# Kernel tuning notes

Measured on AMD Instinct MI355X. Metric: run time of the kernel, lower is better.

Reference implementation:

```python
import jax, jax.numpy as jnp
import numpy as np

N = 50000   # nodes
E = 800000  # edges
IN, H, OUT = 64, 512, 128


def _lin_init(key, out_dim, in_dim):
    kw, kb = jax.random.split(key)
    bound = 1.0 / np.sqrt(in_dim)
    W = jax.random.uniform(kw, (out_dim, in_dim), jnp.float32, -bound, bound)
    b = jax.random.uniform(kb, (out_dim,), jnp.float32, -bound, bound)
    return W, b


def setup_inputs() -> dict:
    key = jax.random.key(0)
    ks = jax.random.split(key, 10)
    x = jax.random.normal(ks[0], (N, IN), jnp.float32)
    edge_index = jax.random.randint(ks[1], (2, E), 0, N, jnp.int64)
    W_s1, b_s1 = _lin_init(ks[2], H, IN)
    W_s2, b_s2 = _lin_init(ks[3], H, H)
    W_s3, b_s3 = _lin_init(ks[4], H, H)
    W_s4, b_s4 = _lin_init(ks[5], H, H)
    W_m1, b_m1 = _lin_init(ks[6], OUT, H)
    W_m2, b_m2 = _lin_init(ks[7], OUT, OUT)
    W_l1, b_l1 = _lin_init(ks[8], OUT, H)
    W_l2, b_l2 = _lin_init(ks[9], OUT, OUT)
    return {"x": x, "edge_index": edge_index,
            "W_s1": W_s1, "b_s1": b_s1, "W_s2": W_s2, "b_s2": b_s2,
            "W_s3": W_s3, "b_s3": b_s3, "W_s4": W_s4, "b_s4": b_s4,
            "W_m1": W_m1, "b_m1": b_m1, "W_m2": W_m2, "b_m2": b_m2,
            "W_l1": W_l1, "b_l1": b_l1, "W_l2": W_l2, "b_l2": b_l2}


def _aggregate(h, src, dst):
    # GINConv with default eps=0: (1+eps)*x + sum_{j in N(i)} x_j
    return h + jax.ops.segment_sum(h[src], dst, num_segments=N)


def reference(x, edge_index,
              W_s1, b_s1, W_s2, b_s2, W_s3, b_s3, W_s4, b_s4,
              W_m1, b_m1, W_m2, b_m2, W_l1, b_l1, W_l2, b_l2):
    src, dst = edge_index[0], edge_index[1]
    lrelu = lambda v: jax.nn.leaky_relu(v, 0.1)

    def mlp_shared(h):
        h = lrelu(h @ W_s1.T + b_s1)
        h = lrelu(h @ W_s2.T + b_s2)
        h = lrelu(h @ W_s3.T + b_s3)
        return h @ W_s4.T + b_s4

    def mlp_mu(h):
        return jax.nn.relu(h @ W_m1.T + b_m1) @ W_m2.T + b_m2

    def mlp_logvar(h):
        return jax.nn.relu(h @ W_l1.T + b_l1) @ W_l2.T + b_l2

    h = jax.nn.relu(mlp_shared(_aggregate(x, src, dst)))
    mu = mlp_mu(_aggregate(h, src, dst))
    logvar = mlp_logvar(_aggregate(h, src, dst))
    return (mu, logvar)
```

## Files before the change

kernel.cpp:

```cpp
#include <hip/hip_runtime.h>
#include <hip/hip_bf16.h>
#include <stdint.h>

#define N_NODES 50000
#define N_PAD   50048
#define E_EDGES 800000
#define MT      391

typedef __bf16 bf16x8 __attribute__((ext_vector_type(8)));
typedef __bf16 bf16x4 __attribute__((ext_vector_type(4)));
typedef float  f32x4  __attribute__((ext_vector_type(4)));

__global__ void count_deg(const int* __restrict__ ei, int* __restrict__ cnt) {
    int e = blockIdx.x * blockDim.x + threadIdx.x;
    if (e < E_EDGES) atomicAdd(&cnt[ei[E_EDGES + e]], 1);
}

#define SCAN_B 1024
__global__ void scan_block(const int* __restrict__ cnt, int* __restrict__ ptr,
                           int* __restrict__ bsum, int n) {
    __shared__ int buf[SCAN_B];
    int i = blockIdx.x * SCAN_B + threadIdx.x;
    int v = (i < n) ? cnt[i] : 0;
    buf[threadIdx.x] = v;
    __syncthreads();
    #pragma unroll
    for (int off = 1; off < SCAN_B; off <<= 1) {
        int t = (threadIdx.x >= (unsigned)off) ? buf[threadIdx.x - off] : 0;
        __syncthreads();
        buf[threadIdx.x] += t;
        __syncthreads();
    }
    if (i < n) ptr[i] = buf[threadIdx.x] - v;
    if (threadIdx.x == SCAN_B - 1) bsum[blockIdx.x] = buf[SCAN_B - 1];
}

__global__ void scan_bsums(const int* __restrict__ bsum, int* __restrict__ boff,
                           int nb, int* __restrict__ total_out) {
    __shared__ int buf[SCAN_B];
    int v = ((int)threadIdx.x < nb) ? bsum[threadIdx.x] : 0;
    buf[threadIdx.x] = v;
    __syncthreads();
    #pragma unroll
    for (int off = 1; off < SCAN_B; off <<= 1) {
        int t = (threadIdx.x >= (unsigned)off) ? buf[threadIdx.x - off] : 0;
        __syncthreads();
        buf[threadIdx.x] += t;
        __syncthreads();
    }
    if ((int)threadIdx.x < nb) boff[threadIdx.x] = buf[threadIdx.x] - v;
    if (threadIdx.x == SCAN_B - 1) *total_out = buf[SCAN_B - 1];
}

__global__ void scan_add(int* __restrict__ ptr, const int* __restrict__ boff, int n) {
    int i = blockIdx.x * SCAN_B + threadIdx.x;
    if (i < n) ptr[i] += boff[blockIdx.x];
}

__global__ void fill_csr(const int* __restrict__ ei, const int* __restrict__ ptr,
                         int* __restrict__ cursor, int* __restrict__ col) {
    int e = blockIdx.x * blockDim.x + threadIdx.x;
    if (e < E_EDGES) {
        int dst = ei[E_EDGES + e];
        int pos = ptr[dst] + atomicAdd(&cursor[dst], 1);
        col[pos] = ei[e];
    }
}

#define XN      3200000
#define WTOT    983040
__global__ void cvt_all(const float* __restrict__ x,
                        const float* __restrict__ Ws1, const float* __restrict__ Ws2,
                        const float* __restrict__ Ws3, const float* __restrict__ Ws4,
                        const float* __restrict__ Wm1, const float* __restrict__ Wl1,
                        const float* __restrict__ Wm2, const float* __restrict__ Wl2,
                        __bf16* __restrict__ xb, __bf16* __restrict__ wbuf) {
    int i = blockIdx.x * blockDim.x + threadIdx.x;
    if (i < XN) { xb[i] = (__bf16)x[i]; return; }
    int j = i - XN;
    if (j >= WTOT) return;
    const float* s; int o;
    if      (j <  32768) { s = Ws1; o = j; }
    else if (j < 294912) { s = Ws2; o = j -  32768; }
    else if (j < 557056) { s = Ws3; o = j - 294912; }
    else if (j < 819200) { s = Ws4; o = j - 557056; }
    else if (j < 884736) { s = Wm1; o = j - 819200; }
    else if (j < 950272) { s = Wl1; o = j - 884736; }
    else if (j < 966656) { s = Wm2; o = j - 950272; }
    else                 { s = Wl2; o = j - 966656; }
    wbuf[j] = (__bf16)s[o];
}

__global__ __launch_bounds__(256) void agg0_gather(
    const __bf16* __restrict__ xb, const int* __restrict__ ptr,
    const int* __restrict__ col, __bf16* __restrict__ out) {
    int node = blockIdx.x * 4 + (threadIdx.x >> 6);
    int lane = threadIdx.x & 63;
    int g    = lane >> 3;
    int f0   = (lane & 7) << 3;
    if (node >= N_PAD) return;
    long o = (long)node * 64 + f0;
    if (node >= N_NODES) {
        if (g == 0) {
            bf16x8 z;
            #pragma unroll
            for (int i = 0; i < 8; ++i) z[i] = (__bf16)0.0f;
            *(bf16x8*)&out[o] = z;
        }
        return;
    }
    float a[8];
    #pragma unroll
    for (int i = 0; i < 8; ++i) a[i] = 0.0f;
    if (g == 0) {
        bf16x8 s = *(const bf16x8*)&xb[o];
        #pragma unroll
        for (int i = 0; i < 8; ++i) a[i] = (float)s[i];
    }
    int e0 = ptr[node], e1 = ptr[node + 1];
    int e = e0;
    for (; e + 16 <= e1; e += 16) {
        int c0 = col[e + g];
        int c1 = col[e + 8 + g];
        bf16x8 v0 = *(const bf16x8*)&xb[(c0 << 6) + f0];
        bf16x8 v1 = *(const bf16x8*)&xb[(c1 << 6) + f0];
        #pragma unroll
        for (int i = 0; i < 8; ++i) a[i] += (float)v0[i] + (float)v1[i];
    }
    int rem = e1 - e;
    if (rem > 0) {
        int u0 = (g < rem) ? g : 0;        float m0 = (g < rem) ? 1.0f : 0.0f;
        int i1 = g + 8;
        int u1 = (i1 < rem) ? i1 : 0;      float m1 = (i1 < rem) ? 1.0f : 0.0f;
        int c0 = col[e + u0];
        int c1 = col[e + u1];
        bf16x8 v0 = *(const bf16x8*)&xb[(c0 << 6) + f0];
        bf16x8 v1 = *(const bf16x8*)&xb[(c1 << 6) + f0];
        #pragma unroll
        for (int i = 0; i < 8; ++i) a[i] += m0 * (float)v0[i] + m1 * (float)v1[i];
    }
    #pragma unroll
    for (int i = 0; i < 8; ++i) {
        a[i] += __shfl_xor(a[i], 8, 64);
        a[i] += __shfl_xor(a[i], 16, 64);
        a[i] += __shfl_xor(a[i], 32, 64);
    }
    if (g == 0) {
        bf16x8 r;
        #pragma unroll
        for (int i = 0; i < 8; ++i) r[i] = (__bf16)a[i];
        *(bf16x8*)&out[o] = r;
    }
}

__global__ __launch_bounds__(256) void aggt_gather(
    const __bf16* __restrict__ t, const int* __restrict__ ptr,
    const int* __restrict__ col, const float* __restrict__ b_m1,
    const float* __restrict__ b_l1, __bf16* __restrict__ p) {
    int node = blockIdx.x * 8 + (threadIdx.x >> 5);
    if (node >= N_NODES) return;
    int hl = threadIdx.x & 31;
    int f0 = hl << 3;
    float a[8];
    {
        bf16x8 s = *(const bf16x8*)&t[((long)node << 8) + f0];
        #pragma unroll
        for (int i = 0; i < 8; ++i) a[i] = (float)s[i];
    }
    int e0 = ptr[node], e1 = ptr[node + 1];
    int e = e0;
    for (; e + 8 <= e1; e += 8) {
        int c[8];
        #pragma unroll
        for (int u = 0; u < 8; ++u) c[u] = col[e + u];
        bf16x8 v[8];
        #pragma unroll
        for (int u = 0; u < 8; ++u) v[u] = *(const bf16x8*)&t[((long)c[u] << 8) + f0];
        #pragma unroll
        for (int u = 0; u < 8; ++u)
            #pragma unroll
            for (int i = 0; i < 8; ++i) a[i] += (float)v[u][i];
    }
    int rem = e1 - e;
    if (rem > 0) {
        #pragma unroll
        for (int u = 0; u < 7; ++u) {
            int   uu = (u < rem) ? u : 0;
            float m  = (u < rem) ? 1.0f : 0.0f;
            int   cc = col[e + uu];
            bf16x8 v = *(const bf16x8*)&t[((long)cc << 8) + f0];
            #pragma unroll
            for (int i = 0; i < 8; ++i) a[i] += m * (float)v[i];
        }
    }
    const float* bp = (f0 < 128) ? (b_m1 + f0) : (b_l1 + (f0 - 128));
    f32x4 b0 = *(const f32x4*)bp;
    f32x4 b1 = *(const f32x4*)(bp + 4);
    bf16x8 r;
    #pragma unroll
    for (int i = 0; i < 4; ++i) r[i]     = (__bf16)fmaxf(a[i]     + b0[i], 0.0f);
    #pragma unroll
    for (int i = 0; i < 4; ++i) r[4 + i] = (__bf16)fmaxf(a[4 + i] + b1[i], 0.0f);
    *(bf16x8*)&p[((long)node << 8) + f0] = r;
}

__device__ __forceinline__ void gl_lds16(const __bf16* g, __bf16* l) {
    __builtin_amdgcn_global_load_lds(
        (const __attribute__((address_space(1))) uint32_t*)g,
        (__attribute__((address_space(3))) uint32_t*)l, 16, 0, 0);
}

__device__ __forceinline__ void stage_w(const __bf16* __restrict__ W, int K, int k0,
                                        __bf16* __restrict__ buf, int nrows,
                                        int wid, int lane) {
    int ipw = nrows >> 7;
    int r16 = lane >> 2, sl = lane & 3;
    #pragma unroll
    for (int i = 0; i < 4; ++i) {
        if (i < ipw) {
            int cc = wid * ipw + i;
            int r  = cc * 16 + r16;
            int kt = sl ^ ((r >> 1) & 3);
            gl_lds16(W + (long)r * K + k0 + kt * 8, buf + cc * 512);
        }
    }
}

template <int NI>
__device__ __forceinline__ void chunk_mfma(const __bf16* __restrict__ sAct,
    const __bf16* __restrict__ buf, int c, int rA, int q, int wncol,
    f32x4 (&acc)[4][NI]) {
    const int g   = c * 4 + q;
    const int sla = ((g & 56) | ((g & 7) ^ (rA & 7))) << 3;
    bf16x8 af[4], bfr[NI];
    #pragma unroll
    for (int mi = 0; mi < 4; ++mi)
        af[mi] = *(const bf16x8*)&sAct[(mi * 16 + rA) * 512 + sla];
    #pragma unroll
    for (int ni = 0; ni < NI; ++ni) {
        int wr = wncol + ni * 16 + rA;
        bfr[ni] = *(const bf16x8*)&buf[wr * 32 + ((q ^ ((wr >> 1) & 3)) << 3)];
    }
    #pragma unroll
    for (int mi = 0; mi < 4; ++mi)
        #pragma unroll
        for (int ni = 0; ni < NI; ++ni)
            acc[mi][ni] = __builtin_amdgcn_mfma_f32_16x16x32_bf16(
                af[mi], bfr[ni], acc[mi][ni], 0, 0, 0);
}

__device__ __forceinline__ void chunk_mfma_a0(const __bf16* __restrict__ act0,
    const __bf16* __restrict__ buf, int c, int rA, int q, int wncol,
    f32x4 (&acc)[4][4]) {
    const int g   = c * 4 + q;
    const int sla = (g ^ (rA & 7)) << 3;
    bf16x8 af[4], bfr[4];
    #pragma unroll
    for (int mi = 0; mi < 4; ++mi)
        af[mi] = *(const bf16x8*)&act0[(mi * 16 + rA) * 64 + sla];
    #pragma unroll
    for (int ni = 0; ni < 4; ++ni) {
        int wr = wncol + ni * 16 + rA;
        bfr[ni] = *(const bf16x8*)&buf[wr * 32 + ((q ^ ((wr >> 1) & 3)) << 3)];
    }
    #pragma unroll
    for (int mi = 0; mi < 4; ++mi)
        #pragma unroll
        for (int ni = 0; ni < 4; ++ni)
            acc[mi][ni] = __builtin_amdgcn_mfma_f32_16x16x32_bf16(
                af[mi], bfr[ni], acc[mi][ni], 0, 0, 0);
}

template <int ACTn>
__device__ __forceinline__ void writeback_act(__bf16* __restrict__ sAct,
    f32x4 (&acc)[4][4], const float* __restrict__ bias,
    int wn, int ccol, int crow) {
    float bv[4];
    #pragma unroll
    for (int ni = 0; ni < 4; ++ni) bv[ni] = bias[wn + ni * 16 + ccol];
    #pragma unroll
    for (int mi = 0; mi < 4; ++mi)
        #pragma unroll
        for (int ni = 0; ni < 4; ++ni) {
            int cc = wn + ni * 16 + ccol;
            int g  = cc >> 3;
            #pragma unroll
            for (int p = 0; p < 4; ++p) {
                int rr = mi * 16 + crow + p;
                float v = acc[mi][ni][p] + bv[ni];
                if (ACTn == 1) v = (v > 0.0f) ? v : 0.1f * v;
                else           v = fmaxf(v, 0.0f);
                int sl = (g & 56) | ((g & 7) ^ (rr & 7));
                sAct[rr * 512 + sl * 8 + (cc & 7)] = (__bf16)v;
            }
        }
}

template <int ACTn>
__device__ __forceinline__ void layer512(__bf16* __restrict__ sAct,
    __bf16* __restrict__ bufA, __bf16* __restrict__ bufB,
    const __bf16* __restrict__ W, const __bf16* __restrict__ Wnext,
    int nrows_next, const float* __restrict__ bias,
    int wn, int rA, int q, int ccol, int crow, int wid, int lane) {
    f32x4 acc[4][4];
    #pragma unroll
    for (int i = 0; i < 4; ++i)
        #pragma unroll
        for (int j = 0; j < 4; ++j) acc[i][j] = (f32x4)0.0f;
    #pragma unroll
    for (int c = 0; c < 16; ++c) {
        if (c < 15) stage_w(W, 512, (c + 1) * 32, (c & 1) ? bufA : bufB, 512, wid, lane);
        else        stage_w(Wnext, 512, 0, bufA, nrows_next, wid, lane);
        chunk_mfma<4>(sAct, (c & 1) ? bufB : bufA, c, rA, q, wn, acc);
        __syncthreads();
    }
    writeback_act<ACTn>(sAct, acc, bias, wn, ccol, crow);
    __syncthreads();
}

__global__ __launch_bounds__(512) void mlp_fused(
    const __bf16* __restrict__ a0,
    const __bf16* __restrict__ w1, const float* __restrict__ b1,
    const __bf16* __restrict__ w2, const float* __restrict__ b2,
    const __bf16* __restrict__ w3, const float* __restrict__ b3,
    const __bf16* __restrict__ w4, const float* __restrict__ b4,
    const __bf16* __restrict__ wp,
    __bf16* __restrict__ tg)
{
    __shared__ __bf16 lds[69632];
    __bf16* act0 = lds;
    __bf16* sAct = lds + 4096;
    __bf16* bufA = lds + 36864;
    __bf16* bufB = lds + 53248;

    const int tid  = threadIdx.x;
    const int wid  = tid >> 6;
    const int lane = tid & 63;
    const long blockRow = (long)blockIdx.x * 64;

    const int rA   = lane & 15;
    const int q    = lane >> 4;
    const int ccol = lane & 15;
    const int crow = (lane >> 4) << 2;
    const int wn   = wid << 6;
    const int wnp  = wid << 5;

    {
        int srow = lane >> 3;
        int skg  = (lane & 7) ^ srow;
        gl_lds16(a0 + (blockRow + wid * 8 + srow) * 64 + skg * 8, act0 + wid * 512);
    }
    stage_w(w1, 64, 0, bufA, 512, wid, lane);
    __syncthreads();

    {
        f32x4 acc[4][4];
        #pragma unroll
        for (int i = 0; i < 4; ++i)
            #pragma unroll
            for (int j = 0; j < 4; ++j) acc[i][j] = (f32x4)0.0f;
        stage_w(w1, 64, 32, bufB, 512, wid, lane);
        chunk_mfma_a0(act0, bufA, 0, rA, q, wn, acc);
        __syncthreads();
        stage_w(w2, 512, 0, bufA, 512, wid, lane);
        chunk_mfma_a0(act0, bufB, 1, rA, q, wn, acc);
        __syncthreads();
        writeback_act<1>(sAct, acc, b1, wn, ccol, crow);
        __syncthreads();
    }

    layer512<1>(sAct, bufA, bufB, w2, w3, 512, b2, wn, rA, q, ccol, crow, wid, lane);
    layer512<1>(sAct, bufA, bufB, w3, w4, 512, b3, wn, rA, q, ccol, crow, wid, lane);
    layer512<2>(sAct, bufA, bufB, w4, wp, 256, b4, wn, rA, q, ccol, crow, wid, lane);

    {
        f32x4 accp[4][2];
        #pragma unroll
        for (int i = 0; i < 4; ++i)
            #pragma unroll
            for (int j = 0; j < 2; ++j) accp[i][j] = (f32x4)0.0f;
        #pragma unroll
        for (int c = 0; c < 16; ++c) {
            if (c < 15) stage_w(wp, 512, (c + 1) * 32, (c & 1) ? bufA : bufB, 256, wid, lane);
            chunk_mfma<2>(sAct, (c & 1) ? bufB : bufA, c, rA, q, wnp, accp);
            __syncthreads();
        }
        #pragma unroll
        for (int mi = 0; mi < 4; ++mi)
            #pragma unroll
            for (int ni = 0; ni < 2; ++ni)
                #pragma unroll
                for (int p = 0; p < 4; ++p)
                    bufA[(mi * 16 + crow + p) * 256 + wnp + ni * 16 + ccol] =
                        (__bf16)accp[mi][ni][p];
        __syncthreads();
        int rr = tid >> 3;
        int c0 = (tid & 7) << 5;
        const bf16x8* s = (const bf16x8*)&bufA[rr * 256 + c0];
        __bf16* d = tg + (blockRow + rr) * 256 + c0;
        #pragma unroll
        for (int i = 0; i < 4; ++i) *(bf16x8*)(d + i * 8) = s[i];
    }
}

template <int NCOL>
__device__ __forceinline__ void swizzle_xy(int bid, int& x, int& y) {
    int grp  = bid / (8 * NCOL);
    int rem  = bid - grp * (8 * NCOL);
    int base = grp * 8;
    int width = MT - base; if (width > 8) width = 8;
    x = base + rem % width;
    y = rem / width;
}

template <int ACT, bool BIAS, bool OUT_BF16, bool MCHK>
__device__ __forceinline__ void gemm_core(
    const __bf16* __restrict__ A, int lda, const __bf16* __restrict__ W,
    const float* __restrict__ bias, void* __restrict__ Cout, int ldc,
    int K, long Mstore, long blockRow, int blockCol,
    __bf16* __restrict__ smem) {
    __bf16* As = smem;
    __bf16* Ws = smem + 8192;
    const int tid  = threadIdx.x;
    const int wid  = tid >> 6;
    const int lane = tid & 63;
    const int wm = (wid >> 1) << 6;
    const int wn = (wid & 1) << 6;

    f32x4 acc[4][4];
    #pragma unroll
    for (int i = 0; i < 4; ++i)
        #pragma unroll
        for (int j = 0; j < 4; ++j) acc[i][j] = (f32x4)0.0f;

    const int srow = lane >> 3;
    const int skg  = (lane & 7) ^ srow;
    const __bf16* gA[4]; const __bf16* gW[4];
    __bf16 *lA[4], *lW[4];
    #pragma unroll
    for (int i = 0; i < 4; ++i) {
        int c = wid * 4 + i;
        gA[i] = A + (blockRow + c * 8 + srow) * (long)lda + skg * 8;
        gW[i] = W + ((long)blockCol + c * 8 + srow) * (long)K + skg * 8;
        lA[i] = As + c * 512;
        lW[i] = Ws + c * 512;
    }

    const int rA = lane & 15;
    const int q  = lane >> 4;
    const int r7 = rA & 7;

    for (int k0 = 0; k0 < K; k0 += 64) {
        #pragma unroll
        for (int i = 0; i < 4; ++i) gl_lds16(gA[i] + k0, lA[i]);
        #pragma unroll
        for (int i = 0; i < 4; ++i) gl_lds16(gW[i] + k0, lW[i]);
        __syncthreads();

        #pragma unroll
        for (int s = 0; s < 2; ++s) {
            const int slot = ((s * 4 + q) ^ r7) * 8;
            bf16x8 af[4], bf[4];
            #pragma unroll
            for (int mi = 0; mi < 4; ++mi)
                af[mi] = *(const bf16x8*)&As[(wm + mi * 16 + rA) * 64 + slot];
            #pragma unroll
            for (int ni = 0; ni < 4; ++ni)
                bf[ni] = *(const bf16x8*)&Ws[(wn + ni * 16 + rA) * 64 + slot];
            #pragma unroll
            for (int mi = 0; mi < 4; ++mi)
                #pragma unroll
                for (int ni = 0; ni < 4; ++ni)
                    acc[mi][ni] = __builtin_amdgcn_mfma_f32_16x16x32_bf16(
                        af[mi], bf[ni], acc[mi][ni], 0, 0, 0);
        }
        __syncthreads();
    }

    const int ccol = lane & 15;
    const int crow = (lane >> 4) << 2;
    if (OUT_BF16 && !MCHK) {
        #pragma unroll
        for (int mi = 0; mi < 4; ++mi) {
            #pragma unroll
            for (int ni = 0; ni < 4; ++ni) {
                int gc = wn + ni * 16 + ccol;
                float bv = BIAS ? bias[blockCol + gc] : 0.0f;
                #pragma unroll
                for (int r = 0; r < 4; ++r) {
                    float v = acc[mi][ni][r] + bv;
                    if (ACT == 1) v = (v > 0.0f) ? v : 0.1f * v;
                    else if (ACT == 2) v = fmaxf(v, 0.0f);
                    smem[(wm + mi * 16 + crow + r) * 128 + gc] = (__bf16)v;
                }
            }
        }
        __syncthreads();
        #pragma unroll
        for (int i = 0; i < 8; ++i) {
            int o   = (i * 256 + tid) * 8;
            int row = o >> 7;
            int co  = o & 127;
            *(bf16x8*)((__bf16*)Cout + (blockRow + row) * (long)ldc + blockCol + co) =
                *(const bf16x8*)&smem[o];
        }
    } else if (!OUT_BF16) {
        float* fsmem = (float*)smem;
        #pragma unroll
        for (int half = 0; half < 2; ++half) {
            __syncthreads();
            if ((wm >> 6) == half) {
                #pragma unroll
                for (int mi = 0; mi < 4; ++mi) {
                    #pragma unroll
                    for (int ni = 0; ni < 4; ++ni) {
                        int gc = wn + ni * 16 + ccol;
                        float bv = BIAS ? bias[blockCol + gc] : 0.0f;
                        #pragma unroll
                        for (int r = 0; r < 4; ++r) {
                            float v = acc[mi][ni][r] + bv;
                            if (ACT == 1) v = (v > 0.0f) ? v : 0.1f * v;
                            else if (ACT == 2) v = fmaxf(v, 0.0f);
                            fsmem[(mi * 16 + crow + r) * 128 + gc] = v;
                        }
                    }
                }
            }
            __syncthreads();
            #pragma unroll
            for (int i = 0; i < 8; ++i) {
                int o   = i * 256 + tid;
                int row = o >> 5;
                int co  = (o & 31) * 4;
                long gr = blockRow + half * 64 + row;
                if (!MCHK || gr < Mstore)
                    *(f32x4*)((float*)Cout + gr * (long)ldc + blockCol + co) =
                        *(const f32x4*)&fsmem[o * 4];
            }
        }
    } else {
        #pragma unroll
        for (int mi = 0; mi < 4; ++mi) {
            #pragma unroll
            for (int ni = 0; ni < 4; ++ni) {
                long gr0 = blockRow + wm + mi * 16 + crow;
                int  gc  = blockCol + wn + ni * 16 + ccol;
                float bv = BIAS ? bias[gc] : 0.0f;
                #pragma unroll
                for (int r = 0; r < 4; ++r) {
                    long gr = gr0 + r;
                    if (!MCHK || gr < Mstore) {
                        float v = acc[mi][ni][r] + bv;
                        if (ACT == 1) v = (v > 0.0f) ? v : 0.1f * v;
                        else if (ACT == 2) v = fmaxf(v, 0.0f);
                        ((__bf16*)Cout)[gr * ldc + gc] = (__bf16)v;
                    }
                }
            }
        }
    }
}

__global__ __launch_bounds__(256) void gemm_heads(
    const __bf16* __restrict__ p, const __bf16* __restrict__ wm2,
    const float* __restrict__ b_m2, float* __restrict__ mu,
    const __bf16* __restrict__ wl2, const float* __restrict__ b_l2,
    float* __restrict__ lv) {
    __shared__ __bf16 smem[128 * 128];
    int x, hd;
    swizzle_xy<2>(blockIdx.x, x, hd);
    if (hd == 0)
        gemm_core<0, true, false, true>(p, 256, wm2, b_m2, mu, 128, 128, N_NODES,
                                        (long)x * 128, 0, smem);
    else
        gemm_core<0, true, false, true>(p + 128, 256, wl2, b_l2, lv, 128, 128, N_NODES,
                                        (long)x * 128, 0, smem);
}

extern "C" void kernel_launch(void* const* d_in, const int* in_sizes, int n_in,
                              void* d_out, int out_size, void* d_ws, size_t ws_size,
                              hipStream_t stream) {
    const float* x    = (const float*)d_in[0];
    const int*   ei   = (const int*)d_in[1];
    const float* W_s1 = (const float*)d_in[2];
    const float* b_s1 = (const float*)d_in[3];
    const float* W_s2 = (const float*)d_in[4];
    const float* b_s2 = (const float*)d_in[5];
    const float* W_s3 = (const float*)d_in[6];
    const float* b_s3 = (const float*)d_in[7];
    const float* W_s4 = (const float*)d_in[8];
    const float* b_s4 = (const float*)d_in[9];
    const float* W_m1 = (const float*)d_in[10];
    const float* b_m1 = (const float*)d_in[11];
    const float* W_m2 = (const float*)d_in[12];
    const float* b_m2 = (const float*)d_in[13];
    const float* W_l1 = (const float*)d_in[14];
    const float* b_l1 = (const float*)d_in[15];
    const float* W_l2 = (const float*)d_in[16];
    const float* b_l2 = (const float*)d_in[17];

    char* ws = (char*)d_ws;
    size_t off = 0;
    auto carve = [&](size_t bytes) -> void* {
        void* p = ws + off;
        off = (off + bytes + 255) & ~(size_t)255;
        return p;
    };
    int* ptr  = (int*)carve((size_t)(N_NODES + 1) * 4);
    int* col  = (int*)carve((size_t)E_EDGES * 4);
    int* bsum = (int*)carve(SCAN_B * 4);
    int* boff = (int*)carve(SCAN_B * 4);
    __bf16* wbuf = (__bf16*)carve((size_t)WTOT * 2);
    __bf16* w1  = wbuf;
    __bf16* w2  = wbuf +  32768;
    __bf16* w3  = wbuf + 294912;
    __bf16* w4  = wbuf + 557056;
    __bf16* wml = wbuf + 819200;
    __bf16* wm2 = wbuf + 950272;
    __bf16* wl2 = wbuf + 966656;
    __bf16* xb    = (__bf16*)carve((size_t)XN * 2);
    __bf16* agg0b = (__bf16*)carve((size_t)N_PAD * 64 * 2);
    __bf16* B1    = (__bf16*)carve((size_t)N_PAD * 512 * 2);
    __bf16* B2    = (__bf16*)carve((size_t)N_PAD * 512 * 2);

    int* cnt = (int*)B1;
    int* cur = (int*)B2;

    (void)hipMemsetAsync(cnt, 0, (size_t)N_NODES * 4, stream);
    (void)hipMemsetAsync(cur, 0, (size_t)N_NODES * 4, stream);

    const int NB = (N_NODES + SCAN_B - 1) / SCAN_B;
    count_deg<<<E_EDGES / 256, 256, 0, stream>>>(ei, cnt);
    scan_block<<<NB, SCAN_B, 0, stream>>>(cnt, ptr, bsum, N_NODES);
    scan_bsums<<<1, SCAN_B, 0, stream>>>(bsum, boff, NB, &ptr[N_NODES]);
    scan_add<<<NB, SCAN_B, 0, stream>>>(ptr, boff, N_NODES);
    fill_csr<<<E_EDGES / 256, 256, 0, stream>>>(ei, ptr, cur, col);

    cvt_all<<<(XN + WTOT + 255) / 256, 256, 0, stream>>>(
        x, W_s1, W_s2, W_s3, W_s4, W_m1, W_l1, W_m2, W_l2, xb, wbuf);

    agg0_gather<<<N_PAD / 4, 256, 0, stream>>>(xb, ptr, col, agg0b);

    __bf16* t = B1;
    mlp_fused<<<N_PAD / 64, 512, 0, stream>>>(agg0b, w1, b_s1, w2, b_s2,
                                              w3, b_s3, w4, b_s4, wml, t);

    __bf16* p = B2;
    aggt_gather<<<(N_NODES + 7) / 8, 256, 0, stream>>>(t, ptr, col, b_m1, b_l1, p);

    float* mu = (float*)d_out;
    float* lv = mu + (size_t)N_NODES * 128;
    gemm_heads<<<MT * 2, 256, 0, stream>>>(p, wm2, b_m2, mu, wl2, b_l2, lv);
}
```

Before: 465.1 us.

## Deepen weight staging pipeline in fused MLP with vmcnt waits

Restructures the fused MLP kernel's weight staging into a two-chunk-ahead pipeline. Explicit s_waitcnt vmcnt counters and raw barriers replace full __syncthreads, so global-to-LDS loads stay in flight across MFMA chunks. The projection layer now stages 64-wide K chunks, giving 8 iterations instead of 16, and biases are preloaded into registers once. This is meant to hide weight-load latency and cut barrier overhead. The cost is fragile hand-managed counter and barrier logic, where a wrong wait count could race.

New measurement: 442.4 us. 1.05x faster.

```diff
diff --git a/kernel.cpp b/kernel.cpp
--- a/kernel.cpp
+++ b/kernel.cpp
@@ -210,41 +210,53 @@
         (__attribute__((address_space(3))) uint32_t*)l, 16, 0, 0);
 }
 
-__device__ __forceinline__ void stage_w(const __bf16* __restrict__ W, int K, int k0,
-                                        __bf16* __restrict__ buf, int nrows,
-                                        int wid, int lane) {
-    int ipw = nrows >> 7;
-    int r16 = lane >> 2, sl = lane & 3;
-    #pragma unroll
-    for (int i = 0; i < 4; ++i) {
-        if (i < ipw) {
-            int cc = wid * ipw + i;
+#define P_WAITN(n) asm volatile("s_waitcnt vmcnt(" #n ")" ::: "memory")
+#define P_LGKM0 asm volatile("s_waitcnt lgkmcnt(0)" ::: "memory")
+#define P_BAR   __builtin_amdgcn_s_barrier()
+
+__device__ __forceinline__ void stage_chunk(const __bf16* __restrict__ W, int Kdim,
+                                            int k0, bool rows512,
+                                            __bf16* __restrict__ buf,
+                                            int wid, int lane) {
+    if (rows512) {
+        int r16 = lane >> 2, sl = lane & 3;
+        #pragma unroll
+        for (int i = 0; i < 4; ++i) {
+            int cc = wid * 4 + i;
             int r  = cc * 16 + r16;
             int kt = sl ^ ((r >> 1) & 3);
-            gl_lds16(W + (long)r * K + k0 + kt * 8, buf + cc * 512);
-        }
-    }
-}
-
-template <int NI>
-__device__ __forceinline__ void chunk_mfma(const __bf16* __restrict__ sAct,
+            gl_lds16(W + (long)r * Kdim + k0 + kt * 8, buf + cc * 512);
+        }
+    } else {
+        int r8 = lane >> 3, sl = lane & 7;
+        #pragma unroll
+        for (int i = 0; i < 4; ++i) {
+            int cc = wid * 4 + i;
+            int r  = cc * 8 + r8;
+            int kt = sl ^ (r & 7);
+            gl_lds16(W + (long)r * Kdim + k0 + kt * 8, buf + cc * 512);
+        }
+    }
+}
+
+__device__ __forceinline__ void chunk_mfma4(const __bf16* __restrict__ sAct,
     const __bf16* __restrict__ buf, int c, int rA, int q, int wncol,
-    f32x4 (&acc)[4][NI]) {
+    f32x4 (&acc)[4][4]) {
     const int g   = c * 4 + q;
     const int sla = ((g & 56) | ((g & 7) ^ (rA & 7))) << 3;
-    bf16x8 af[4], bfr[NI];
+    bf16x8 af[4], bfr[4];
     #pragma unroll
     for (int mi = 0; mi < 4; ++mi)
         af[mi] = *(const bf16x8*)&sAct[(mi * 16 + rA) * 512 + sla];
     #pragma unroll
-    for (int ni = 0; ni < NI; ++ni) {
+    for (int ni = 0; ni < 4; ++ni) {
         int wr = wncol + ni * 16 + rA;
         bfr[ni] = *(const bf16x8*)&buf[wr * 32 + ((q ^ ((wr >> 1) & 3)) << 3)];
     }
     #pragma unroll
     for (int mi = 0; mi < 4; ++mi)
         #pragma unroll
-        for (int ni = 0; ni < NI; ++ni)
+        for (int ni = 0; ni < 4; ++ni)
             acc[mi][ni] = __builtin_amdgcn_mfma_f32_16x16x32_bf16(
                 af[mi], bfr[ni], acc[mi][ni], 0, 0, 0);
 }
@@ -271,13 +283,36 @@
                 af[mi], bfr[ni], acc[mi][ni], 0, 0, 0);
 }
 
+__device__ __forceinline__ void chunk_mfma_proj(const __bf16* __restrict__ sAct,
+    const __bf16* __restrict__ buf, int c, int rA, int q, int wnp,
+    f32x4 (&accp)[4][2]) {
+    #pragma unroll
+    for (int s = 0; s < 2; ++s) {
+        const int g   = c * 8 + s * 4 + q;
+        const int sla = ((g & 56) | ((g & 7) ^ (rA & 7))) << 3;
+        bf16x8 af[4], bfr[2];
+        #pragma unroll
+        for (int mi = 0; mi < 4; ++mi)
+            af[mi] = *(const bf16x8*)&sAct[(mi * 16 + rA) * 512 + sla];
+        #pragma unroll
+        for (int ni = 0; ni < 2; ++ni) {
+            int wr = wnp + ni * 16 + rA;
+            int gB = s * 4 + q;
+            bfr[ni] = *(const bf16x8*)&buf[wr * 64 + ((gB ^ (wr & 7)) << 3)];
+        }
+        #pragma unroll
+        for (int mi = 0; mi < 4; ++mi)
+            #pragma unroll
+            for (int ni = 0; ni < 2; ++ni)
+                accp[mi][ni] = __builtin_amdgcn_mfma_f32_16x16x32_bf16(
+                    af[mi], bfr[ni], accp[mi][ni], 0, 0, 0);
+    }
+}
+
 template <int ACTn>
 __device__ __forceinline__ void writeback_act(__bf16* __restrict__ sAct,
-    f32x4 (&acc)[4][4], const float* __restrict__ bias,
+    f32x4 (&acc)[4][4], const float* __restrict__ bv,
     int wn, int ccol, int crow) {
-    float bv[4];
-    #pragma unroll
-    for (int ni = 0; ni < 4; ++ni) bv[ni] = bias[wn + ni * 16 + ccol];
     #pragma unroll
     for (int mi = 0; mi < 4; ++mi)
         #pragma unroll
@@ -297,10 +332,11 @@
 }
 
 template <int ACTn>
-__device__ __forceinline__ void layer512(__bf16* __restrict__ sAct,
-    __bf16* __restrict__ bufA, __bf16* __restrict__ bufB,
-    const __bf16* __restrict__ W, const __bf16* __restrict__ Wnext,
-    int nrows_next, const float* __restrict__ bias,
+__device__ __forceinline__ void layer512_pipe(
+    __bf16* __restrict__ sAct, __bf16* __restrict__ s0, __bf16* __restrict__ s1,
+    const __bf16* __restrict__ W,
+    const __bf16* __restrict__ Wn, int Kn, bool n512, int k0n_c1,
+    const float* __restrict__ bv,
     int wn, int rA, int q, int ccol, int crow, int wid, int lane) {
     f32x4 acc[4][4];
     #pragma unroll
@@ -309,13 +345,20 @@
         for (int j = 0; j < 4; ++j) acc[i][j] = (f32x4)0.0f;
     #pragma unroll
     for (int c = 0; c < 16; ++c) {
-        if (c < 15) stage_w(W, 512, (c + 1) * 32, (c & 1) ? bufA : bufB, 512, wid, lane);
-        else        stage_w(Wnext, 512, 0, bufA, nrows_next, wid, lane);
-        chunk_mfma<4>(sAct, (c & 1) ? bufB : bufA, c, rA, q, wn, acc);
-        __syncthreads();
-    }
-    writeback_act<ACTn>(sAct, acc, bias, wn, ccol, crow);
-    __syncthreads();
+        __bf16* cur = (c & 1) ? s1 : s0;
+        P_WAITN(4); P_BAR;
+        chunk_mfma4(sAct, cur, c, rA, q, wn, acc);
+        if (c < 15) {
+            P_LGKM0; P_BAR;
+            if (c <= 13) stage_chunk(W, 512, (c + 2) * 32, true, cur, wid, lane);
+            else         stage_chunk(Wn, Kn, 0, n512, s0, wid, lane);
+        } else {
+            P_LGKM0; P_BAR;
+            writeback_act<ACTn>(sAct, acc, bv, wn, ccol, crow);
+            __syncthreads();
+            stage_chunk(Wn, Kn, k0n_c1, n512, s1, wid, lane);
+        }
+    }
 }
 
 __global__ __launch_bounds__(512) void mlp_fused(
@@ -330,8 +373,8 @@
     __shared__ __bf16 lds[69632];
     __bf16* act0 = lds;
     __bf16* sAct = lds + 4096;
-    __bf16* bufA = lds + 36864;
-    __bf16* bufB = lds + 53248;
+    __bf16* s0   = lds + 36864;
+    __bf16* s1   = lds + 53248;
 
     const int tid  = threadIdx.x;
     const int wid  = tid >> 6;
@@ -345,13 +388,20 @@
     const int wn   = wid << 6;
     const int wnp  = wid << 5;
 
+    float bv1[4], bv2[4], bv3[4], bv4[4];
+    #pragma unroll
+    for (int ni = 0; ni < 4; ++ni) {
+        int idx = wn + ni * 16 + ccol;
+        bv1[ni] = b1[idx]; bv2[ni] = b2[idx]; bv3[ni] = b3[idx]; bv4[ni] = b4[idx];
+    }
+
     {
         int srow = lane >> 3;
         int skg  = (lane & 7) ^ srow;
         gl_lds16(a0 + (blockRow + wid * 8 + srow) * 64 + skg * 8, act0 + wid * 512);
     }
-    stage_w(w1, 64, 0, bufA, 512, wid, lane);
-    __syncthreads();
+    stage_chunk(w1, 64, 0,  true, s0, wid, lane);
+    stage_chunk(w1, 64, 32, true, s1, wid, lane);
 
     {
         f32x4 acc[4][4];
@@ -359,19 +409,20 @@
         for (int i = 0; i < 4; ++i)
             #pragma unroll
             for (int j = 0; j < 4; ++j) acc[i][j] = (f32x4)0.0f;
-        stage_w(w1, 64, 32, bufB, 512, wid, lane);
-        chunk_mfma_a0(act0, bufA, 0, rA, q, wn, acc);
-        __syncthreads();
-        stage_w(w2, 512, 0, bufA, 512, wid, lane);
-        chunk_mfma_a0(act0, bufB, 1, rA, q, wn, acc);
-        __syncthreads();
-        writeback_act<1>(sAct, acc, b1, wn, ccol, crow);
-        __syncthreads();
-    }
-
-    layer512<1>(sAct, bufA, bufB, w2, w3, 512, b2, wn, rA, q, ccol, crow, wid, lane);
-    layer512<1>(sAct, bufA, bufB, w3, w4, 512, b3, wn, rA, q, ccol, crow, wid, lane);
-    layer512<2>(sAct, bufA, bufB, w4, wp, 256, b4, wn, rA, q, ccol, crow, wid, lane);
+        P_WAITN(4); P_BAR;
+        chunk_mfma_a0(act0, s0, 0, rA, q, wn, acc);
+        P_LGKM0; P_BAR;
+        stage_chunk(w2, 512, 0, true, s0, wid, lane);
+        P_WAITN(4); P_BAR;
+        chunk_mfma_a0(act0, s1, 1, rA, q, wn, acc);
+        writeback_act<1>(sAct, acc, bv1, wn, ccol, crow);
+        __syncthreads();
+        stage_chunk(w2, 512, 32, true, s1, wid, lane);
+    }
+
+    layer512_pipe<1>(sAct, s0, s1, w2, w3, 512, true, 32, bv2, wn, rA, q, ccol, crow, wid, lane);
+    layer512_pipe<1>(sAct, s0, s1, w3, w4, 512, true, 32, bv3, wn, rA, q, ccol, crow, wid, lane);
+    layer512_pipe<2>(sAct, s0, s1, w4, wp, 512, false, 64, bv4, wn, rA, q, ccol, crow, wid, lane);
 
     {
         f32x4 accp[4][2];
@@ -380,10 +431,13 @@
             #pragma unroll
             for (int j = 0; j < 2; ++j) accp[i][j] = (f32x4)0.0f;
         #pragma unroll
-        for (int c = 0; c < 16; ++c) {
-            if (c < 15) stage_w(wp, 512, (c + 1) * 32, (c & 1) ? bufA : bufB, 256, wid, lane);
-            chunk_mfma<2>(sAct, (c & 1) ? bufB : bufA, c, rA, q, wnp, accp);
-            __syncthreads();
+        for (int c = 0; c < 8; ++c) {
+            __bf16* cur = (c & 1) ? s1 : s0;
+            if (c == 7) { P_WAITN(0); } else { P_WAITN(4); }
+            P_BAR;
+            chunk_mfma_proj(sAct, cur, c, rA, q, wnp, accp);
+            P_LGKM0; P_BAR;
+            if (c < 6) stage_chunk(wp, 512, (c + 2) * 64, false, cur, wid, lane);
         }
         #pragma unroll
         for (int mi = 0; mi < 4; ++mi)
@@ -391,12 +445,12 @@
             for (int ni = 0; ni < 2; ++ni)
                 #pragma unroll
                 for (int p = 0; p < 4; ++p)
-                    bufA[(mi * 16 + crow + p) * 256 + wnp + ni * 16 + ccol] =
+                    s0[(mi * 16 + crow + p) * 256 + wnp + ni * 16 + ccol] =
                         (__bf16)accp[mi][ni][p];
         __syncthreads();
         int rr = tid >> 3;
         int c0 = (tid & 7) << 5;
-        const bf16x8* s = (const bf16x8*)&bufA[rr * 256 + c0];
+        const bf16x8* s = (const bf16x8*)&s0[rr * 256 + c0];
         __bf16* d = tg + (blockRow + rr) * 256 + c0;
         #pragma unroll
         for (int i = 0; i < 4; ++i) *(bf16x8*)(d + i * 8) = s[i];
```
